# Optimization experiments

Measured on AMD Instinct MI355X. Metric: run time of the kernel, lower is better.

Reference implementation:

```python
import jax, jax.numpy as jnp
jax.config.update("jax_enable_x64", True)
import numpy as np

BUCKETS = 2147483647  # max int32, as in fused_project call sites
HALF = BUCKETS >> 1
NGRAM_SIZE = 3
# sgnn partition boundaries: indices = [i*(i+1)/2 * P for i in range(n)] + [proj], P=112
IDX = [0, 112, 336, 672]


def _project(sig, mask, seeds):
    """One SgnnProjection partition.

    sig:   [B, M] int64 hash signatures in [0, BUCKETS) (padded ragged rows)
    mask:  [B, M] bool validity of each padded slot (ragged row structure)
    seeds: [H] int64 hash seeds
    returns [B, H] float32
    """
    # value = floormod(abs(sig * seed), buckets); center to [-half, half]
    v = jnp.abs(sig[None, :, :] * seeds[:, None, None]) % BUCKETS  # [H, B, M]
    v = v - jnp.where(v > HALF, BUCKETS, 0)
    vf = v.astype(jnp.float32) * mask[None].astype(jnp.float32)
    counts = jnp.maximum(mask.sum(-1), 1).astype(jnp.float32)  # [B], ragged row lengths
    mean = vf.sum(-1) / counts[None]  # [H, B]  (ragged reduce_mean)
    return (mean / HALF).T  # [B, H]


def setup_inputs() -> dict:
    key = jax.random.key(0)
    k1, k2, k3 = jax.random.split(key, 3)
    signatures = jax.random.randint(k1, (NGRAM_SIZE, 1024, 128), 0, BUCKETS, dtype=jnp.int64)
    mask = jax.random.bernoulli(k2, 0.7, (NGRAM_SIZE, 1024, 128))
    hash_seed = jax.random.randint(k3, (IDX[-1],), 1, BUCKETS, dtype=jnp.int64)
    return {"signatures": signatures, "mask": mask, "hash_seed": hash_seed}


def reference(signatures, mask, hash_seed):
    outs = [
        _project(signatures[i], mask[i], hash_seed[IDX[i]:IDX[i + 1]])
        for i in range(NGRAM_SIZE)
    ]
    return jnp.concatenate(outs, axis=-1).astype(jnp.float32)  # [B, 672]
```

## Files before the change

kernel.cpp:

```cpp
#include <hip/hip_runtime.h>


#define M31    2147483647u
#define HALF_B 1073741823u

__device__ __forceinline__ unsigned relem(unsigned v, unsigned long long seed) {
    const unsigned long long p2 = (unsigned long long)v * seed + (unsigned long long)HALF_B;
    const unsigned lo = (unsigned)p2;
    const unsigned hi = (unsigned)(p2 >> 32);
    const unsigned s  = __builtin_amdgcn_alignbit(hi, lo, 31) + (lo & 0x7FFFFFFFu);
    return min(s, s - M31);
}

__global__ __launch_bounds__(704) void sgnn_fused2_kernel(
    const int* __restrict__ sig,
    const int* __restrict__ mask,
    const int* __restrict__ seeds,
    float* __restrict__ out,
    int nbatch)
{
    __shared__ unsigned srow[2][3][128];
    __shared__ float    sinv[2][3];
    __shared__ unsigned scnt[2][3];

    const unsigned tid  = threadIdx.x;
    const unsigned lane = tid & 63u;
    const unsigned W    = tid >> 6;
    const unsigned b0   = blockIdx.x << 1;

    if (W < 6u) {
        const unsigned rr   = W & 1u;
        const unsigned pp   = W >> 1;
        const unsigned brow = b0 + rr;
        if (brow < (unsigned)nbatch) {
            const unsigned base = (pp * (unsigned)nbatch + brow) * 128u + lane * 2u;
            const int2 sg = *(const int2*)&sig[base];
            const int2 mk = *(const int2*)&mask[base];

            const unsigned long long bx = __ballot(mk.x != 0);
            const unsigned long long by = __ballot(mk.y != 0);
            const unsigned long long lt = (1ULL << lane) - 1ULL;
            const unsigned cx   = (unsigned)__popcll(bx);
            const unsigned cnt  = cx + (unsigned)__popcll(by);
            if (mk.x) srow[rr][pp][(unsigned)__popcll(bx & lt)]      = (unsigned)sg.x;
            if (mk.y) srow[rr][pp][cx + (unsigned)__popcll(by & lt)] = (unsigned)sg.y;
            if (cnt + lane < 128u)        srow[rr][pp][cnt + lane]        = 0u;
            if (cnt + 64u + lane < 128u)  srow[rr][pp][cnt + 64u + lane]  = 0u;

            if (lane == 0) {
                const unsigned c = cnt ? cnt : 1u;
                sinv[rr][pp] = 1.0f / ((float)c * 1073741823.0f);
                scnt[rr][pp] = cnt;
            }
        }
    }
    __syncthreads();

    const unsigned h     = tid;
    const bool     valid = (h < 672u);
    const unsigned h_c   = valid ? h : 671u;
    const unsigned p     = (h_c < 112u) ? 0u : (h_c < 336u) ? 1u : 2u;

    const unsigned wh0 = tid & ~63u;
    const unsigned wh1 = (wh0 + 63u < 671u) ? wh0 + 63u : 671u;
    const unsigned plo = (wh0 < 112u) ? 0u : (wh0 < 336u) ? 1u : 2u;
    const unsigned phi = (wh1 < 112u) ? 0u : (wh1 < 336u) ? 1u : 2u;

    const unsigned long long seed = (unsigned long long)(unsigned)seeds[h_c];

#pragma unroll
    for (unsigned r = 0; r < 2u; ++r) {
        const unsigned brow = b0 + r;
        if (brow < (unsigned)nbatch) {
            unsigned nmax = max(scnt[r][plo], scnt[r][phi]);
            nmax = (nmax + 7u) & ~7u;
            nmax = __builtin_amdgcn_readfirstlane(nmax);

            const unsigned* __restrict__ rp = srow[r][p];

            unsigned long long sum0 = 0, sum1 = 0;
            for (unsigned mm = 0; mm < nmax; mm += 8u) {
                const uint4 a = *(const uint4*)&rp[mm];
                const uint4 c = *(const uint4*)&rp[mm + 4u];
                sum0 += (unsigned long long)(relem(a.x, seed) + relem(a.y, seed));
                sum1 += (unsigned long long)(relem(a.z, seed) + relem(a.w, seed));
                sum0 += (unsigned long long)(relem(c.x, seed) + relem(c.y, seed));
                sum1 += (unsigned long long)(relem(c.z, seed) + relem(c.w, seed));
            }

            if (valid) {
                const long long centered = (long long)(sum0 + sum1)
                                         - (long long)nmax * 1073741823LL;
                out[brow * 672u + h] = (float)centered * sinv[r][p];
            }
        }
    }
}

extern "C" void kernel_launch(void* const* d_in, const int* in_sizes, int n_in,
                              void* d_out, int out_size, void* d_ws, size_t ws_size,
                              hipStream_t stream) {
    const int* sig   = (const int*)d_in[0];
    const int* mask  = (const int*)d_in[1];
    const int* seeds = (const int*)d_in[2];
    float* out = (float*)d_out;

    const int nbatch = in_sizes[0] / (3 * 128);
    const int nblk   = (nbatch + 1) / 2;
    sgnn_fused2_kernel<<<dim3(nblk), dim3(704), 0, stream>>>(sig, mask, seeds, out, nbatch);
}
```

Before: 74.73 us.

## Split work into 3 column chunks per batch row with 256-thread blocks

Replaces the 704-thread block that handled two batch rows and all 672 outputs with a 2D grid of (3 column chunks × batch) blocks of 256 threads. Each block computes 224 outputs and compacts only the one or two partitions it needs into shared memory. The smaller blocks and launch bounds aim for higher occupancy and better load balance across CUs. The cost is more blocks, repeated staging of rows shared by adjacent chunks, and 32 idle threads per block.

```diff
diff --git a/kernel.cpp b/kernel.cpp
--- a/kernel.cpp
+++ b/kernel.cpp
@@ -12,88 +12,80 @@
     return min(s, s - M31);
 }
 
-__global__ __launch_bounds__(704) void sgnn_fused2_kernel(
+__global__ __launch_bounds__(256, 8) void sgnn_hocc_kernel(
     const int* __restrict__ sig,
     const int* __restrict__ mask,
     const int* __restrict__ seeds,
     float* __restrict__ out,
     int nbatch)
 {
-    __shared__ unsigned srow[2][3][128];
-    __shared__ float    sinv[2][3];
-    __shared__ unsigned scnt[2][3];
+    __shared__ unsigned srow[2][128];
+    __shared__ float    sinv[2];
+    __shared__ unsigned scnt[2];
 
     const unsigned tid  = threadIdx.x;
     const unsigned lane = tid & 63u;
     const unsigned W    = tid >> 6;
-    const unsigned b0   = blockIdx.x << 1;
+    const unsigned c    = blockIdx.x;
+    const unsigned b    = blockIdx.y;
 
-    if (W < 6u) {
-        const unsigned rr   = W & 1u;
-        const unsigned pp   = W >> 1;
-        const unsigned brow = b0 + rr;
-        if (brow < (unsigned)nbatch) {
-            const unsigned base = (pp * (unsigned)nbatch + brow) * 128u + lane * 2u;
-            const int2 sg = *(const int2*)&sig[base];
-            const int2 mk = *(const int2*)&mask[base];
+    if (W < 2u && c + W < 3u) {
+        const unsigned p    = c + W;
+        const unsigned base = (p * (unsigned)nbatch + b) * 128u + lane * 2u;
+        const int2 sg = *(const int2*)&sig[base];
+        const int2 mk = *(const int2*)&mask[base];
 
-            const unsigned long long bx = __ballot(mk.x != 0);
-            const unsigned long long by = __ballot(mk.y != 0);
-            const unsigned long long lt = (1ULL << lane) - 1ULL;
-            const unsigned cx   = (unsigned)__popcll(bx);
-            const unsigned cnt  = cx + (unsigned)__popcll(by);
-            if (mk.x) srow[rr][pp][(unsigned)__popcll(bx & lt)]      = (unsigned)sg.x;
-            if (mk.y) srow[rr][pp][cx + (unsigned)__popcll(by & lt)] = (unsigned)sg.y;
-            if (cnt + lane < 128u)        srow[rr][pp][cnt + lane]        = 0u;
-            if (cnt + 64u + lane < 128u)  srow[rr][pp][cnt + 64u + lane]  = 0u;
+        const unsigned long long bx = __ballot(mk.x != 0);
+        const unsigned long long by = __ballot(mk.y != 0);
+        const unsigned long long lt = (1ULL << lane) - 1ULL;
+        const unsigned cx   = (unsigned)__popcll(bx);
+        const unsigned cnt  = cx + (unsigned)__popcll(by);
+        if (mk.x) srow[W][(unsigned)__popcll(bx & lt)]      = (unsigned)sg.x;
+        if (mk.y) srow[W][cx + (unsigned)__popcll(by & lt)] = (unsigned)sg.y;
+        if (cnt + lane < 128u)        srow[W][cnt + lane]        = 0u;
+        if (cnt + 64u + lane < 128u)  srow[W][cnt + 64u + lane]  = 0u;
 
-            if (lane == 0) {
-                const unsigned c = cnt ? cnt : 1u;
-                sinv[rr][pp] = 1.0f / ((float)c * 1073741823.0f);
-                scnt[rr][pp] = cnt;
-            }
+        if (lane == 0) {
+            const unsigned cc = cnt ? cnt : 1u;
+            sinv[W] = 1.0f / ((float)cc * 1073741823.0f);
+            scnt[W] = cnt;
         }
     }
     __syncthreads();
 
-    const unsigned h     = tid;
-    const bool     valid = (h < 672u);
-    const unsigned h_c   = valid ? h : 671u;
-    const unsigned p     = (h_c < 112u) ? 0u : (h_c < 336u) ? 1u : 2u;
+    const bool     valid = (tid < 224u);
+    const unsigned ht    = valid ? tid : 223u;
+    const unsigned h     = 224u * c + ht;
+    const unsigned p     = (h < 112u) ? 0u : (h < 336u) ? 1u : 2u;
+    const unsigned lp    = p - c;
 
-    const unsigned wh0 = tid & ~63u;
-    const unsigned wh1 = (wh0 + 63u < 671u) ? wh0 + 63u : 671u;
-    const unsigned plo = (wh0 < 112u) ? 0u : (wh0 < 336u) ? 1u : 2u;
-    const unsigned phi = (wh1 < 112u) ? 0u : (wh1 < 336u) ? 1u : 2u;
+    const unsigned e0  = tid & ~63u;
+    const unsigned e1  = (e0 + 63u < 223u) ? e0 + 63u : 223u;
+    const unsigned g0  = 224u * c + e0;
+    const unsigned g1  = 224u * c + e1;
+    const unsigned plo = (g0 < 112u) ? 0u : (g0 < 336u) ? 1u : 2u;
+    const unsigned phi = (g1 < 112u) ? 0u : (g1 < 336u) ? 1u : 2u;
+    unsigned nmax = max(scnt[plo - c], scnt[phi - c]);
+    nmax = (nmax + 7u) & ~7u;
+    nmax = __builtin_amdgcn_readfirstlane(nmax);
 
-    const unsigned long long seed = (unsigned long long)(unsigned)seeds[h_c];
+    const unsigned long long seed = (unsigned long long)(unsigned)seeds[h];
+    const unsigned* __restrict__ rp = srow[lp];
 
-#pragma unroll
-    for (unsigned r = 0; r < 2u; ++r) {
-        const unsigned brow = b0 + r;
-        if (brow < (unsigned)nbatch) {
-            unsigned nmax = max(scnt[r][plo], scnt[r][phi]);
-            nmax = (nmax + 7u) & ~7u;
-            nmax = __builtin_amdgcn_readfirstlane(nmax);
+    unsigned long long sum0 = 0, sum1 = 0;
+    for (unsigned mm = 0; mm < nmax; mm += 8u) {
+        const uint4 a = *(const uint4*)&rp[mm];
+        const uint4 q = *(const uint4*)&rp[mm + 4u];
+        sum0 += (unsigned long long)(relem(a.x, seed) + relem(a.y, seed));
+        sum1 += (unsigned long long)(relem(a.z, seed) + relem(a.w, seed));
+        sum0 += (unsigned long long)(relem(q.x, seed) + relem(q.y, seed));
+        sum1 += (unsigned long long)(relem(q.z, seed) + relem(q.w, seed));
+    }
 
-            const unsigned* __restrict__ rp = srow[r][p];
-
-            unsigned long long sum0 = 0, sum1 = 0;
-            for (unsigned mm = 0; mm < nmax; mm += 8u) {
-                const uint4 a = *(const uint4*)&rp[mm];
-                const uint4 c = *(const uint4*)&rp[mm + 4u];
-                sum0 += (unsigned long long)(relem(a.x, seed) + relem(a.y, seed));
-                sum1 += (unsigned long long)(relem(a.z, seed) + relem(a.w, seed));
-                sum0 += (unsigned long long)(relem(c.x, seed) + relem(c.y, seed));
-                sum1 += (unsigned long long)(relem(c.z, seed) + relem(c.w, seed));
-            }
-
-            if (valid) {
-                const long long centered = (long long)(sum0 + sum1)
-                                         - (long long)nmax * 1073741823LL;
-                out[brow * 672u + h] = (float)centered * sinv[r][p];
-            }
-        }
+    if (valid) {
+        const long long centered = (long long)(sum0 + sum1)
+                                 - (long long)nmax * 1073741823LL;
+        out[b * 672u + h] = (float)centered * sinv[lp];
     }
 }
 
@@ -106,6 +98,5 @@
     float* out = (float*)d_out;
 
     const int nbatch = in_sizes[0] / (3 * 128);
-    const int nblk   = (nbatch + 1) / 2;
-    sgnn_fused2_kernel<<<dim3(nblk), dim3(704), 0, stream>>>(sig, mask, seeds, out, nbatch);
+    sgnn_hocc_kernel<<<dim3(3, nbatch), dim3(256), 0, stream>>>(sig, mask, seeds, out, nbatch);
 }
```

Measured after the change: 74.33 us. Within noise of the previous version (-0.5%).
